# Optimization experiments

Measured on AMD Instinct MI355X. Metric: run time of the kernel, lower is better.

Reference implementation:

```python
import jax, jax.numpy as jnp
import numpy as np

KWTA = 16          # number of winners (kwta)
THRESH = 16384.0   # firing threshold


def setup_inputs() -> dict:
    key = jax.random.key(0)
    k1, k2 = jax.random.split(key)
    # SpykeTorch layout: (timesteps, in_channels, H, W)
    rec_field = jax.random.uniform(k1, (64, 1, 256, 256), dtype=jnp.float32)
    # LocalConvolution weight: kernel covers the full receptive field -> (k, C, kh, kw)
    weight = jax.random.uniform(k2, (2048, 1, 256, 256), dtype=jnp.float32)
    return {"rec_field": rec_field, "weight": weight}


def reference(rec_field, weight):
    T = rec_field.shape[0]
    K = weight.shape[0]
    # LocalConvolution with kernel == receptive field: output spatial dims are 1x1,
    # i.e. a dense projection of the flattened field onto K cells -> (T, K)
    out = jnp.einsum('tchw,kchw->tk', rec_field, weight)
    # sf.fire(out, thresh, True): threshold_ keeps values strictly > thresh, else 0
    pot = jnp.where(out > THRESH, out, jnp.zeros((), out.dtype))  # thresholded potentials
    spikes = jnp.sign(pot)                                        # 0/1 spike wave
    # sf.get_k_winners(pot, kwta, inhibition_radius=0); spikes = pot.sign()
    n_spk = spikes.sum(axis=0)                                    # (K,)
    # index of earliest spike timestep per feature, clamped to [0, T-1]
    first_idx = jnp.clip((T - n_spk).astype(jnp.int32), 0, T - 1)
    first_pot = jnp.take_along_axis(pot, first_idx[None, :], axis=0)  # (1, K)
    trunc = spikes * first_pot                                    # (T, K)
    v = trunc.max() * T                                           # large bias at spike positions
    total = (trunc + spikes * v).sum(axis=0)                      # (K,) ranking score
    # iterative argmax + zeroing of the winning feature (radius 0) == top-k,
    # with the loop's break-on-zero handled by the validity mask
    top_vals, top_idx = jax.lax.top_k(total, KWTA)
    valid = (top_vals > 0).astype(out.dtype)
    coef = jnp.zeros((K,), dtype=out.dtype).at[top_idx].set(valid)  # winner channel mask
    # coef broadcast over timesteps; restore (T, K, 1, 1) spatial layout
    return jnp.sign(pot * coef[None, :])[:, :, None, None]
```

## Files before the change

kernel.cpp:

```cpp
#include <hip/hip_runtime.h>


typedef float  f32x4  __attribute__((ext_vector_type(4)));
typedef __bf16 bf16x8 __attribute__((ext_vector_type(8)));
typedef short  s16x8  __attribute__((ext_vector_type(8)));

constexpr int KDIM   = 65536;
constexpr int NCOL   = 2048;
constexpr int TROWS  = 64;
constexpr int CTILE  = 64;
constexpr int KS     = 64;
constexpr int SPLIT  = 16;
constexpr int KRANGE = KDIM / SPLIT;
constexpr int STAGES = KRANGE / KS;
constexpr int LDSTR  = 72;
constexpr long long THRESH_I = 1LL << 60;

__device__ __forceinline__ void convert_write16(const float4 v[4], short* base) {
    const int PST = TROWS * LDSTR;
    ushort h[3][16];
#pragma unroll
    for (int i = 0; i < 16; ++i) {
        const float     x  = ((const float*)v)[i];
        const unsigned  k  = (unsigned)(x * 8388608.0f);
        const int       d0 = (int)((k + 128u) & 255u) - 128;
        const unsigned  k1 = (k - (unsigned)d0) >> 8;
        const int       d1 = (int)((k1 + 128u) & 255u) - 128;
        const unsigned  k2 = (k1 - (unsigned)d1) >> 8;
        h[0][i] = (ushort)(__float_as_uint((float)d0) >> 16);
        h[1][i] = (ushort)(__float_as_uint((float)d1) >> 16);
        h[2][i] = (ushort)(__float_as_uint((float)(int)k2) >> 16);
    }
#pragma unroll
    for (int p = 0; p < 3; ++p) {
        s16x8 lo, hi;
#pragma unroll
        for (int j = 0; j < 8; ++j) { lo[j] = (short)h[p][j]; hi[j] = (short)h[p][j + 8]; }
        *(s16x8*)(base + p * PST)     = lo;
        *(s16x8*)(base + p * PST + 8) = hi;
    }
}

__global__ __launch_bounds__(256, 2) void gemm_limb(const float* __restrict__ A,
                                                    const float* __restrict__ W,
                                                    unsigned long long* __restrict__ C) {
    __shared__ short Al[3][TROWS][LDSTR];
    __shared__ short Wl[3][CTILE][LDSTR];
    const int tid  = threadIdx.x;
    const int lane = tid & 63;
    const int wv   = tid >> 6;
    const int r0   = (wv >> 1) * 32;
    const int c0   = (wv & 1) * 32;
    const int colBase = blockIdx.x * CTILE;
    const int kBase   = blockIdx.y * KRANGE;

    const int lrow  = tid >> 2;
    const int lkoff = (tid & 3) * 16;

    const int frow = lane & 15;
    const int fk   = (lane >> 4) * 8;

    f32x4 acc[5][2][2] = {};
    long long tot[2][2][4] = {};

    for (int st = 0; st < STAGES; ++st) {
        const int k0 = kBase + st * KS;
        float4 av[4], wv4[4];
        const float* ap = A + (size_t)lrow * KDIM + k0 + lkoff;
        const float* wp = W + (size_t)(colBase + lrow) * KDIM + k0 + lkoff;
#pragma unroll
        for (int i = 0; i < 4; ++i) av[i] = ((const float4*)ap)[i];
#pragma unroll
        for (int i = 0; i < 4; ++i) wv4[i] = ((const float4*)wp)[i];

        __syncthreads();
        convert_write16(av,  &Al[0][lrow][lkoff]);
        convert_write16(wv4, &Wl[0][lrow][lkoff]);
        __syncthreads();

#pragma unroll
        for (int ks = 0; ks < 2; ++ks) {
            s16x8 af[3][2], bf[3][2];
#pragma unroll
            for (int p = 0; p < 3; ++p)
#pragma unroll
                for (int rt = 0; rt < 2; ++rt)
                    af[p][rt] = *(const s16x8*)&Al[p][r0 + rt * 16 + frow][ks * 32 + fk];
#pragma unroll
            for (int p = 0; p < 3; ++p)
#pragma unroll
                for (int ct = 0; ct < 2; ++ct)
                    bf[p][ct] = *(const s16x8*)&Wl[p][c0 + ct * 16 + frow][ks * 32 + fk];
#pragma unroll
            for (int p = 0; p < 3; ++p)
#pragma unroll
                for (int q = 0; q < 3; ++q) {
                    const int s = p + q;
#pragma unroll
                    for (int rt = 0; rt < 2; ++rt)
#pragma unroll
                        for (int ct = 0; ct < 2; ++ct)
                            acc[s][rt][ct] = __builtin_amdgcn_mfma_f32_16x16x32_bf16(
                                __builtin_bit_cast(bf16x8, af[p][rt]),
                                __builtin_bit_cast(bf16x8, bf[q][ct]),
                                acc[s][rt][ct], 0, 0, 0);
                }
        }

        if ((st & 3) == 3) {
#pragma unroll
            for (int s = 0; s < 5; ++s)
#pragma unroll
                for (int rt = 0; rt < 2; ++rt)
#pragma unroll
                    for (int ct = 0; ct < 2; ++ct) {
#pragma unroll
                        for (int r = 0; r < 4; ++r)
                            tot[rt][ct][r] += ((long long)(int)acc[s][rt][ct][r]) << (8 * s);
                        acc[s][rt][ct] = (f32x4){0.f, 0.f, 0.f, 0.f};
                    }
        }
    }

#pragma unroll
    for (int rt = 0; rt < 2; ++rt)
#pragma unroll
        for (int ct = 0; ct < 2; ++ct)
#pragma unroll
            for (int r = 0; r < 4; ++r) {
                const int row = r0 + rt * 16 + (lane >> 4) * 4 + r;
                const int col = colBase + c0 + ct * 16 + (lane & 15);
                atomicAdd(&C[(size_t)row * NCOL + col],
                          (unsigned long long)tot[rt][ct][r]);
            }
}

__global__ __launch_bounds__(256) void colstats(const long long* __restrict__ C,
                                                int* __restrict__ nspk,
                                                long long* __restrict__ fpot,
                                                unsigned long long* __restrict__ mbits) {
    const int k = blockIdx.x * blockDim.x + threadIdx.x;
    int n = 0;
    for (int t = 0; t < TROWS; ++t) n += (C[(size_t)t * NCOL + k] > THRESH_I) ? 1 : 0;
    int fi = TROWS - n;
    if (fi > TROWS - 1) fi = TROWS - 1;
    const long long c  = C[(size_t)fi * NCOL + k];
    const long long fp = (c > THRESH_I) ? c : 0;
    nspk[k] = n;
    fpot[k] = fp;
    atomicMax(mbits, (unsigned long long)fp);
}

__global__ __launch_bounds__(256) void topk16(const long long* __restrict__ fpot,
                                              const int* __restrict__ nspk,
                                              const unsigned long long* __restrict__ mbits,
                                              unsigned int* __restrict__ coef) {
    __shared__ long long sf[NCOL];
    __shared__ int sn[NCOL];
    __shared__ long long rv[256];
    __shared__ int rn[256];
    __shared__ int ri[256];
    const int tid = threadIdx.x;
    const bool anyv = (*mbits) > 0ull;
    for (int k = tid; k < NCOL; k += 256) { sf[k] = fpot[k]; sn[k] = nspk[k]; }
    __syncthreads();

    for (int round = 0; round < 16; ++round) {
        int bn = -1; long long bf = -1; int bi = 1 << 30;
        for (int k = tid; k < NCOL; k += 256) {
            const int nn = sn[k]; const long long ff = sf[k];
            if (nn > bn || (nn == bn && (ff > bf || (ff == bf && k < bi)))) {
                bn = nn; bf = ff; bi = k;
            }
        }
        rn[tid] = bn; rv[tid] = bf; ri[tid] = bi;
        __syncthreads();
        for (int s = 128; s > 0; s >>= 1) {
            if (tid < s) {
                const int on = rn[tid + s]; const long long of = rv[tid + s]; const int oi = ri[tid + s];
                if (on > rn[tid] || (on == rn[tid] && (of > rv[tid] || (of == rv[tid] && oi < ri[tid])))) {
                    rn[tid] = on; rv[tid] = of; ri[tid] = oi;
                }
            }
            __syncthreads();
        }
        if (tid == 0) {
            const int w = ri[0];
            if (rn[0] > 0 && anyv) coef[w] = 1u;
            sn[w] = -1;
        }
        __syncthreads();
    }
}

__global__ __launch_bounds__(256) void writeout(const long long* __restrict__ C,
                                                const unsigned int* __restrict__ coef,
                                                float* __restrict__ out) {
    const int idx = blockIdx.x * blockDim.x + threadIdx.x;
    const int k = idx & (NCOL - 1);
    out[idx] = (coef[k] != 0u && C[idx] > THRESH_I) ? 1.0f : 0.0f;
}

extern "C" void kernel_launch(void* const* d_in, const int* in_sizes, int n_in,
                              void* d_out, int out_size, void* d_ws, size_t ws_size,
                              hipStream_t stream) {
    (void)in_sizes; (void)n_in; (void)out_size; (void)ws_size;
    const float* A = (const float*)d_in[0];
    const float* W = (const float*)d_in[1];
    float* out = (float*)d_out;

    char* ws = (char*)d_ws;
    long long* Cacc = (long long*)ws;
    unsigned long long* mbits = (unsigned long long*)(ws + 1048576);
    unsigned int* coef = (unsigned int*)(ws + 1048576 + 8);
    long long* fpot = (long long*)(ws + 1048576 + 8 + 8192);
    int* nspk = (int*)(ws + 1048576 + 8 + 8192 + 16384);
    const size_t zero_bytes = 1048576 + 8 + 8192;

    hipMemsetAsync(d_ws, 0, zero_bytes, stream);

    gemm_limb<<<dim3(NCOL / CTILE, SPLIT), 256, 0, stream>>>(
        A, W, (unsigned long long*)Cacc);
    colstats<<<NCOL / 256, 256, 0, stream>>>(Cacc, nspk, fpot, mbits);
    topk16<<<1, 256, 0, stream>>>(fpot, nspk, mbits, coef);
    writeout<<<(TROWS * NCOL) / 256, 256, 0, stream>>>(Cacc, coef, out);
}
```

Baseline: 849.1 us.

## Switch exact limb GEMM from bf16 MFMA to int8 MFMA with offset correction

Replaces the bf16 three-limb decomposition with unsigned byte limbs, shifted to signed int8 by XOR with 0x80, and multiplied via i32 16x16x64 int8 MFMA. Row sums of A and W are accumulated so the offset bias can be removed later in colstats and writeout. This halves the MFMA count per K element, removes the float conversion work and the periodic float-to-int flushes, and packs bytes with perm instructions. The risk is int32 accumulator overflow across the whole K range and added correction arithmetic in the consumer kernels.

```diff
diff --git a/kernel.cpp b/kernel.cpp
--- a/kernel.cpp
+++ b/kernel.cpp
@@ -1,125 +1,115 @@
 #include <hip/hip_runtime.h>
 
 
-typedef float  f32x4  __attribute__((ext_vector_type(4)));
-typedef __bf16 bf16x8 __attribute__((ext_vector_type(8)));
-typedef short  s16x8  __attribute__((ext_vector_type(8)));
+typedef int i32x4 __attribute__((ext_vector_type(4)));
 
 constexpr int KDIM   = 65536;
 constexpr int NCOL   = 2048;
 constexpr int TROWS  = 64;
-constexpr int CTILE  = 64;
-constexpr int KS     = 64;
 constexpr int SPLIT  = 16;
 constexpr int KRANGE = KDIM / SPLIT;
+constexpr int KS     = 64;
 constexpr int STAGES = KRANGE / KS;
-constexpr int LDSTR  = 72;
+constexpr int LROWB  = 80;
+constexpr int PSTB   = TROWS * LROWB;
 constexpr long long THRESH_I = 1LL << 60;
-
-__device__ __forceinline__ void convert_write16(const float4 v[4], short* base) {
-    const int PST = TROWS * LDSTR;
-    ushort h[3][16];
-#pragma unroll
-    for (int i = 0; i < 16; ++i) {
-        const float     x  = ((const float*)v)[i];
-        const unsigned  k  = (unsigned)(x * 8388608.0f);
-        const int       d0 = (int)((k + 128u) & 255u) - 128;
-        const unsigned  k1 = (k - (unsigned)d0) >> 8;
-        const int       d1 = (int)((k1 + 128u) & 255u) - 128;
-        const unsigned  k2 = (k1 - (unsigned)d1) >> 8;
-        h[0][i] = (ushort)(__float_as_uint((float)d0) >> 16);
-        h[1][i] = (ushort)(__float_as_uint((float)d1) >> 16);
-        h[2][i] = (ushort)(__float_as_uint((float)(int)k2) >> 16);
-    }
-#pragma unroll
-    for (int p = 0; p < 3; ++p) {
-        s16x8 lo, hi;
-#pragma unroll
-        for (int j = 0; j < 8; ++j) { lo[j] = (short)h[p][j]; hi[j] = (short)h[p][j + 8]; }
-        *(s16x8*)(base + p * PST)     = lo;
-        *(s16x8*)(base + p * PST + 8) = hi;
-    }
-}
-
-__global__ __launch_bounds__(256, 2) void gemm_limb(const float* __restrict__ A,
-                                                    const float* __restrict__ W,
-                                                    unsigned long long* __restrict__ C) {
-    __shared__ short Al[3][TROWS][LDSTR];
-    __shared__ short Wl[3][CTILE][LDSTR];
+constexpr unsigned long long C_OFF = 8421504ull;
+constexpr unsigned long long C2T   = 65536ull * C_OFF * C_OFF;
+
+__device__ __forceinline__ void cvt4(const float4 f, unsigned& p0, unsigned& p1,
+                                     unsigned& p2, unsigned& s4) {
+    const unsigned k0 = (unsigned)(f.x * 8388608.0f);
+    const unsigned k1 = (unsigned)(f.y * 8388608.0f);
+    const unsigned k2 = (unsigned)(f.z * 8388608.0f);
+    const unsigned k3 = (unsigned)(f.w * 8388608.0f);
+    s4 = k0 + k1 + k2 + k3;
+    unsigned a01, a23;
+    a01 = __builtin_amdgcn_perm(k1, k0, 0x0c0c0400u);
+    a23 = __builtin_amdgcn_perm(k3, k2, 0x0c0c0400u);
+    p0  = __builtin_amdgcn_perm(a23, a01, 0x05040100u) ^ 0x80808080u;
+    a01 = __builtin_amdgcn_perm(k1, k0, 0x0c0c0501u);
+    a23 = __builtin_amdgcn_perm(k3, k2, 0x0c0c0501u);
+    p1  = __builtin_amdgcn_perm(a23, a01, 0x05040100u) ^ 0x80808080u;
+    a01 = __builtin_amdgcn_perm(k1, k0, 0x0c0c0602u);
+    a23 = __builtin_amdgcn_perm(k3, k2, 0x0c0c0602u);
+    p2  = __builtin_amdgcn_perm(a23, a01, 0x05040100u) ^ 0x80808080u;
+}
+
+__global__ __launch_bounds__(256, 2) void gemm_i8(const float* __restrict__ A,
+                                                  const float* __restrict__ W,
+                                                  unsigned long long* __restrict__ P,
+                                                  unsigned long long* __restrict__ Ra,
+                                                  unsigned long long* __restrict__ Sw) {
+    __shared__ char Al[3 * PSTB];
+    __shared__ char Wl[3 * PSTB];
     const int tid  = threadIdx.x;
     const int lane = tid & 63;
     const int wv   = tid >> 6;
     const int r0   = (wv >> 1) * 32;
     const int c0   = (wv & 1) * 32;
-    const int colBase = blockIdx.x * CTILE;
+    const int colBase = blockIdx.x * 64;
     const int kBase   = blockIdx.y * KRANGE;
 
-    const int lrow  = tid >> 2;
-    const int lkoff = (tid & 3) * 16;
+    const int lrow = tid >> 2;
+    const int cch  = (tid & 3) * 16;
 
     const int frow = lane & 15;
-    const int fk   = (lane >> 4) * 8;
-
-    f32x4 acc[5][2][2] = {};
-    long long tot[2][2][4] = {};
+    const int fkB  = (lane >> 4) * 16;
+
+    i32x4 acc[5][2][2] = {};
+    unsigned long long sumA = 0, sumW = 0;
 
     for (int st = 0; st < STAGES; ++st) {
         const int k0 = kBase + st * KS;
         float4 av[4], wv4[4];
-        const float* ap = A + (size_t)lrow * KDIM + k0 + lkoff;
-        const float* wp = W + (size_t)(colBase + lrow) * KDIM + k0 + lkoff;
+        const float* ap = A + (size_t)lrow * KDIM + k0 + cch;
+        const float* wp = W + (size_t)(colBase + lrow) * KDIM + k0 + cch;
 #pragma unroll
         for (int i = 0; i < 4; ++i) av[i] = ((const float4*)ap)[i];
 #pragma unroll
         for (int i = 0; i < 4; ++i) wv4[i] = ((const float4*)wp)[i];
 
-        __syncthreads();
-        convert_write16(av,  &Al[0][lrow][lkoff]);
-        convert_write16(wv4, &Wl[0][lrow][lkoff]);
-        __syncthreads();
-
-#pragma unroll
-        for (int ks = 0; ks < 2; ++ks) {
-            s16x8 af[3][2], bf[3][2];
-#pragma unroll
-            for (int p = 0; p < 3; ++p)
+        unsigned pa[3][4], pw[3][4], sA = 0, sW = 0, s4;
+#pragma unroll
+        for (int g = 0; g < 4; ++g) { cvt4(av[g],  pa[0][g], pa[1][g], pa[2][g], s4); sA += s4; }
+#pragma unroll
+        for (int g = 0; g < 4; ++g) { cvt4(wv4[g], pw[0][g], pw[1][g], pw[2][g], s4); sW += s4; }
+        sumA += sA; sumW += sW;
+
+        __syncthreads();
+#pragma unroll
+        for (int p = 0; p < 3; ++p) {
+            *(i32x4*)(Al + p * PSTB + lrow * LROWB + cch) =
+                (i32x4){(int)pa[p][0], (int)pa[p][1], (int)pa[p][2], (int)pa[p][3]};
+            *(i32x4*)(Wl + p * PSTB + lrow * LROWB + cch) =
+                (i32x4){(int)pw[p][0], (int)pw[p][1], (int)pw[p][2], (int)pw[p][3]};
+        }
+        __syncthreads();
+
+        i32x4 af[3][2], bf[3][2];
+#pragma unroll
+        for (int p = 0; p < 3; ++p)
+#pragma unroll
+            for (int rt = 0; rt < 2; ++rt)
+                af[p][rt] = *(const i32x4*)(Al + p * PSTB + (r0 + rt * 16 + frow) * LROWB + fkB);
+#pragma unroll
+        for (int p = 0; p < 3; ++p)
+#pragma unroll
+            for (int ct = 0; ct < 2; ++ct)
+                bf[p][ct] = *(const i32x4*)(Wl + p * PSTB + (c0 + ct * 16 + frow) * LROWB + fkB);
+
+#pragma unroll
+        for (int p = 0; p < 3; ++p)
+#pragma unroll
+            for (int q = 0; q < 3; ++q) {
+                const int s = p + q;
 #pragma unroll
                 for (int rt = 0; rt < 2; ++rt)
-                    af[p][rt] = *(const s16x8*)&Al[p][r0 + rt * 16 + frow][ks * 32 + fk];
-#pragma unroll
-            for (int p = 0; p < 3; ++p)
-#pragma unroll
-                for (int ct = 0; ct < 2; ++ct)
-                    bf[p][ct] = *(const s16x8*)&Wl[p][c0 + ct * 16 + frow][ks * 32 + fk];
-#pragma unroll
-            for (int p = 0; p < 3; ++p)
-#pragma unroll
-                for (int q = 0; q < 3; ++q) {
-                    const int s = p + q;
-#pragma unroll
-                    for (int rt = 0; rt < 2; ++rt)
-#pragma unroll
-                        for (int ct = 0; ct < 2; ++ct)
-                            acc[s][rt][ct] = __builtin_amdgcn_mfma_f32_16x16x32_bf16(
-                                __builtin_bit_cast(bf16x8, af[p][rt]),
-                                __builtin_bit_cast(bf16x8, bf[q][ct]),
-                                acc[s][rt][ct], 0, 0, 0);
-                }
-        }
-
-        if ((st & 3) == 3) {
-#pragma unroll
-            for (int s = 0; s < 5; ++s)
-#pragma unroll
-                for (int rt = 0; rt < 2; ++rt)
-#pragma unroll
-                    for (int ct = 0; ct < 2; ++ct) {
-#pragma unroll
-                        for (int r = 0; r < 4; ++r)
-                            tot[rt][ct][r] += ((long long)(int)acc[s][rt][ct][r]) << (8 * s);
-                        acc[s][rt][ct] = (f32x4){0.f, 0.f, 0.f, 0.f};
-                    }
-        }
+#pragma unroll
+                    for (int ct = 0; ct < 2; ++ct)
+                        acc[s][rt][ct] = __builtin_amdgcn_mfma_i32_16x16x64_i8(
+                            af[p][rt], bf[q][ct], acc[s][rt][ct], 0, 0, 0);
+            }
     }
 
 #pragma unroll
@@ -128,23 +118,39 @@
         for (int ct = 0; ct < 2; ++ct)
 #pragma unroll
             for (int r = 0; r < 4; ++r) {
+                long long t = 0;
+#pragma unroll
+                for (int s = 0; s < 5; ++s)
+                    t += ((long long)acc[s][rt][ct][r]) << (8 * s);
                 const int row = r0 + rt * 16 + (lane >> 4) * 4 + r;
                 const int col = colBase + c0 + ct * 16 + (lane & 15);
-                atomicAdd(&C[(size_t)row * NCOL + col],
-                          (unsigned long long)tot[rt][ct][r]);
-            }
-}
-
-__global__ __launch_bounds__(256) void colstats(const long long* __restrict__ C,
+                atomicAdd(&P[(size_t)row * NCOL + col], (unsigned long long)t);
+            }
+
+    sumA += __shfl_down(sumA, 2); sumA += __shfl_down(sumA, 1);
+    sumW += __shfl_down(sumW, 2); sumW += __shfl_down(sumW, 1);
+    if ((tid & 3) == 0) {
+        atomicAdd(&Sw[colBase + lrow], sumW);
+        if (blockIdx.x == 0) atomicAdd(&Ra[lrow], sumA);
+    }
+}
+
+__global__ __launch_bounds__(256) void colstats(const unsigned long long* __restrict__ P,
+                                                const unsigned long long* __restrict__ Ra,
+                                                const unsigned long long* __restrict__ Sw,
                                                 int* __restrict__ nspk,
                                                 long long* __restrict__ fpot,
                                                 unsigned long long* __restrict__ mbits) {
     const int k = blockIdx.x * blockDim.x + threadIdx.x;
+    const unsigned long long swk = Sw[k];
     int n = 0;
-    for (int t = 0; t < TROWS; ++t) n += (C[(size_t)t * NCOL + k] > THRESH_I) ? 1 : 0;
+    for (int t = 0; t < TROWS; ++t) {
+        const long long v = (long long)(P[(size_t)t * NCOL + k] + C_OFF * (Ra[t] + swk) - C2T);
+        n += (v > THRESH_I) ? 1 : 0;
+    }
     int fi = TROWS - n;
     if (fi > TROWS - 1) fi = TROWS - 1;
-    const long long c  = C[(size_t)fi * NCOL + k];
+    const long long c  = (long long)(P[(size_t)fi * NCOL + k] + C_OFF * (Ra[fi] + swk) - C2T);
     const long long fp = (c > THRESH_I) ? c : 0;
     nspk[k] = n;
     fpot[k] = fp;
@@ -193,12 +199,16 @@
     }
 }
 
-__global__ __launch_bounds__(256) void writeout(const long long* __restrict__ C,
+__global__ __launch_bounds__(256) void writeout(const unsigned long long* __restrict__ P,
+                                                const unsigned long long* __restrict__ Ra,
+                                                const unsigned long long* __restrict__ Sw,
                                                 const unsigned int* __restrict__ coef,
                                                 float* __restrict__ out) {
     const int idx = blockIdx.x * blockDim.x + threadIdx.x;
+    const int t = idx >> 11;
     const int k = idx & (NCOL - 1);
-    out[idx] = (coef[k] != 0u && C[idx] > THRESH_I) ? 1.0f : 0.0f;
+    const long long v = (long long)(P[idx] + C_OFF * (Ra[t] + Sw[k]) - C2T);
+    out[idx] = (coef[k] != 0u && v > THRESH_I) ? 1.0f : 0.0f;
 }
 
 extern "C" void kernel_launch(void* const* d_in, const int* in_sizes, int n_in,
@@ -210,18 +220,19 @@
     float* out = (float*)d_out;
 
     char* ws = (char*)d_ws;
-    long long* Cacc = (long long*)ws;
+    unsigned long long* P     = (unsigned long long*)ws;
     unsigned long long* mbits = (unsigned long long*)(ws + 1048576);
-    unsigned int* coef = (unsigned int*)(ws + 1048576 + 8);
-    long long* fpot = (long long*)(ws + 1048576 + 8 + 8192);
-    int* nspk = (int*)(ws + 1048576 + 8 + 8192 + 16384);
-    const size_t zero_bytes = 1048576 + 8 + 8192;
+    unsigned int*       coef  = (unsigned int*)(ws + 1048576 + 8);
+    unsigned long long* Ra    = (unsigned long long*)(ws + 1048576 + 8 + 8192);
+    unsigned long long* Sw    = (unsigned long long*)(ws + 1048576 + 8 + 8192 + 512);
+    long long* fpot = (long long*)(ws + 1048576 + 8 + 8192 + 512 + 16384);
+    int*       nspk = (int*)(ws + 1048576 + 8 + 8192 + 512 + 16384 + 16384);
+    const size_t zero_bytes = 1048576 + 8 + 8192 + 512 + 16384;
 
     hipMemsetAsync(d_ws, 0, zero_bytes, stream);
 
-    gemm_limb<<<dim3(NCOL / CTILE, SPLIT), 256, 0, stream>>>(
-        A, W, (unsigned long long*)Cacc);
-    colstats<<<NCOL / 256, 256, 0, stream>>>(Cacc, nspk, fpot, mbits);
+    gemm_i8<<<dim3(NCOL / 64, SPLIT), 256, 0, stream>>>(A, W, P, Ra, Sw);
+    colstats<<<NCOL / 256, 256, 0, stream>>>(P, Ra, Sw, nspk, fpot, mbits);
     topk16<<<1, 256, 0, stream>>>(fpot, nspk, mbits, coef);
-    writeout<<<(TROWS * NCOL) / 256, 256, 0, stream>>>(Cacc, coef, out);
-}
+    writeout<<<(TROWS * NCOL) / 256, 256, 0, stream>>>(P, Ra, Sw, coef, out);
+}
```

After: 783.4 us. 1.08x faster.
